# Kernel tuning notes

Measured on AMD Instinct MI355X. Metric: run time of the kernel, lower is better.

The kernel has to match this reference:

```python
import jax, jax.numpy as jnp
import numpy as np

B, N, FEAT, HID, OUT = 128, 64, 4, 256, 4
E = N * (N - 1)  # fully-connected graph, no self-loops


def _onehot_rel():
    # off-diagonal (recv, send) pairs, matching NRI's encode_onehot construction
    recv, send = np.where(~np.eye(N, dtype=bool))
    rel_rec = np.eye(N, dtype=np.float32)[recv]   # [E, N]
    rel_send = np.eye(N, dtype=np.float32)[send]  # [E, N]
    return jnp.asarray(rel_rec), jnp.asarray(rel_send)


def setup_inputs() -> dict:
    key = jax.random.key(0)
    ks = jax.random.split(key, 8)
    rel_rec, rel_send = _onehot_rel()

    def xavier(k, shape):
        fan_in, fan_out = shape
        lim = (6.0 / (fan_in + fan_out)) ** 0.5
        return jax.random.uniform(k, shape, jnp.float32, -lim, lim)

    return {
        "inputs": jax.random.normal(ks[0], (B, N, FEAT), jnp.float32),
        "edges": jax.random.normal(ks[1], (B, E, 2), jnp.float32),  # unused by forward (as in source)
        "rel_rec": rel_rec,
        "rel_send": rel_send,
        "W_msg1": xavier(ks[2], (2 * FEAT, HID)), "b_msg1": jnp.zeros((HID,), jnp.float32),
        "W_msg2": xavier(ks[3], (HID, HID)),      "b_msg2": jnp.zeros((HID,), jnp.float32),
        "W_out1": xavier(ks[4], (FEAT + HID, HID)), "b_out1": jnp.zeros((HID,), jnp.float32),
        "W_out2": xavier(ks[5], (HID, HID)),      "b_out2": jnp.zeros((HID,), jnp.float32),
        "W_out3": xavier(ks[6], (HID, OUT)),      "b_out3": jnp.zeros((OUT,), jnp.float32),
    }


def reference(inputs, edges, rel_rec, rel_send,
              W_msg1, b_msg1, W_msg2, b_msg2,
              W_out1, b_out1, W_out2, b_out2, W_out3, b_out3):
    x = inputs.reshape(inputs.shape[0], inputs.shape[1], -1)  # [B, N, F]
    # gather node features to edges via one-hot matmuls (faithful to source)
    receivers = jnp.einsum('en,bnf->bef', rel_rec, x)   # [B, E, F]
    senders = jnp.einsum('en,bnf->bef', rel_send, x)    # [B, E, F]
    pre_msg = jnp.concatenate([receivers, senders], axis=-1)  # [B, E, 2F]
    # edge MLP (dropout_prob = 0.0 -> identity)
    msg = jax.nn.relu(pre_msg @ W_msg1 + b_msg1)
    msg = jax.nn.relu(msg @ W_msg2 + b_msg2)            # [B, E, HID]
    # scatter-aggregate back to nodes via rel_rec^T
    agg_msg = jnp.einsum('en,beh->bnh', rel_rec, msg)   # [B, N, HID]
    out = jnp.concatenate([x, agg_msg], axis=-1)        # [B, N, F+HID]
    out = jax.nn.relu(out @ W_out1 + b_out1)
    out = jax.nn.relu(out @ W_out2 + b_out2)
    out = out @ W_out3 + b_out3                          # [B, N, 4]
    return out
```

## Files before the change

kernel.cpp:

```cpp
#include <hip/hip_runtime.h>
#include <cstddef>

typedef _Float16 f16_t;
typedef _Float16 f16x8 __attribute__((ext_vector_type(8)));
typedef float    f32x4  __attribute__((ext_vector_type(4)));
typedef float    f32x16 __attribute__((ext_vector_type(16)));

static constexpr int NN = 64;
static constexpr int FF = 4;
static constexpr int HH = 256;


__device__ inline void pack_frag16(const float* __restrict__ src, f16_t* __restrict__ dst,
                                   int fid, int ksteps, int mode)
{
    if (fid >= ksteps * 1024) return;
    int lane = fid & 63;
    int nt   = (fid >> 6) & 15;
    int ks   = fid >> 10;
    int col  = nt * 16 + (lane & 15);
    int kb   = ks * 32 + (lane >> 4) * 8;
    #pragma unroll
    for (int j = 0; j < 8; ++j) {
        int k = kb + j;
        float v;
        if (mode == 0) {
            v = src[k * 256 + col];
        } else {
            if (k < 256)      v = src[(4 + k) * 256 + col];
            else if (k < 260) v = src[(k - 256) * 256 + col];
            else              v = 0.f;
        }
        dst[(size_t)fid * 8 + j] = (f16_t)v;
    }
}

__device__ inline void pack_frag32(const float* __restrict__ src, f16_t* __restrict__ dst,
                                   int fid)
{
    int lane = fid & 63;
    int nt   = (fid >> 6) & 7;
    int ks   = fid >> 9;
    int col  = nt * 32 + (lane & 31);
    int kb   = ks * 16 + (lane >> 5) * 8;
    #pragma unroll
    for (int j = 0; j < 8; ++j)
        dst[(size_t)fid * 8 + j] = (f16_t)src[(kb + j) * 256 + col];
}

__global__ void prep_all(const float* __restrict__ x,
                         const float* __restrict__ W_msg1,
                         const float* __restrict__ W_msg2,
                         const float* __restrict__ W_out1,
                         const float* __restrict__ W_out2,
                         f16_t* __restrict__ W2p, f16_t* __restrict__ W1op,
                         f16_t* __restrict__ W2op, f16_t* __restrict__ Vp)
{
    int bid = blockIdx.x, tid = threadIdx.x;
    if (bid < 32) {
        pack_frag32(W_msg2, W2p, bid * 256 + tid);
    } else if (bid < 68) {
        pack_frag16(W_out1, W1op, (bid - 32) * 256 + tid, 9, 1);
    } else if (bid < 100) {
        pack_frag16(W_out2, W2op, (bid - 68) * 256 + tid, 8, 0);
    } else {
        int gid  = (bid - 100) * 256 + tid;
        int rown = gid >> 5;
        int h0   = (gid & 31) * 8;
        float4 xv = ((const float4*)x)[rown];
        f16x8 o;
        #pragma unroll
        for (int u = 0; u < 8; ++u) {
            float s = xv.x * W_msg1[4 * HH + h0 + u] + xv.y * W_msg1[5 * HH + h0 + u]
                    + xv.z * W_msg1[6 * HH + h0 + u] + xv.w * W_msg1[7 * HH + h0 + u];
            o[u] = (f16_t)s;
        }
        *(f16x8*)(Vp + (size_t)rown * HH + h0) = o;
    }
}

__global__ __launch_bounds__(256, 2) void edge_kernel(
    const float* __restrict__ x,
    const float* __restrict__ W1,
    const float* __restrict__ b1,
    const f16_t* __restrict__ Vp,
    const f16_t* __restrict__ W2p,
    const float* __restrict__ b2,
    f16_t* __restrict__ innode)
{
    __shared__ __align__(16) char h1[128 * 512];
    __shared__ __align__(16) f16_t Utab[2][256];

    const int tid  = threadIdx.x;
    const int lane = tid & 63;
    const int w    = tid >> 6;
    const int b    = blockIdx.x >> 5;
    const int pr   = blockIdx.x & 31;
    const int i0   = pr * 2, i1 = i0 + 1;

    #pragma unroll
    for (int i = 0; i < 2; ++i) {
        int e    = tid + i * 256;
        int rs   = e >> 8;
        int h    = e & 255;
        int node = rs ? i1 : i0;
        const float* xr = x + (b * NN + node) * FF;
        float s = b1[h] + xr[0] * W1[h] + xr[1] * W1[HH + h]
                        + xr[2] * W1[2 * HH + h] + xr[3] * W1[3 * HH + h];
        Utab[rs][h] = (f16_t)s;
    }
    if (tid < 64) {
        int node = (tid < 32) ? i0 : i1;
        int c = tid & 31;
        float v = (c < 4) ? x[(b * NN + node) * FF + c] : 0.f;
        innode[(size_t)(b * NN + node) * 288 + 256 + c] = (f16_t)v;
    }
    __syncthreads();

    {
        const int hb = tid & 31;
        const int rg = tid >> 5;
        const int h0 = hb * 8;
        const int recv = (rg < 4) ? i0 : i1;
        const f16x8 fz = {};
        f16x8 u8 = *(const f16x8*)&Utab[rg >> 2][h0];
        const int j0 = (rg & 3) * 16;
        const f16x8* vrow = (const f16x8*)(Vp + (size_t)(b * NN + j0) * HH + h0);
        #pragma unroll
        for (int k = 0; k < 16; ++k) {
            int r = rg * 16 + k;
            f16x8 v8 = vrow[k * (HH / 8)];
            f16x8 hv = __builtin_elementwise_max(u8 + v8, fz);
            *(f16x8*)(h1 + r * 512 + (((hb ^ (r & 31)) & 31) << 4)) = hv;
        }
        if ((rg & 3) == (recv >> 4)) {
            int r = rg * 16 + (recv & 15);
            *(f16x8*)(h1 + r * 512 + (((hb ^ (r & 31)) & 31) << 4)) = fz;
        }
    }
    __syncthreads();

    const int ln = lane & 31;
    const int kh = lane >> 5;
    const int wn = w;

    float b2v[2];
    #pragma unroll
    for (int nt = 0; nt < 2; ++nt) b2v[nt] = b2[(wn * 2 + nt) * 32 + ln];

    f32x16 acc[4][2];
    #pragma unroll
    for (int mt = 0; mt < 4; ++mt)
        #pragma unroll
        for (int nt = 0; nt < 2; ++nt)
            #pragma unroll
            for (int e = 0; e < 16; ++e) acc[mt][nt][e] = b2v[nt];

    #pragma unroll
    for (int ks = 0; ks < 16; ++ks) {
        f16x8 bb[2];
        #pragma unroll
        for (int nt = 0; nt < 2; ++nt)
            bb[nt] = *(const f16x8*)(W2p + (size_t)((ks * 8 + wn * 2 + nt) * 64 + lane) * 8);
        #pragma unroll
        for (int mt = 0; mt < 4; ++mt) {
            int row = mt * 32 + ln;
            int c16 = (ks * 2 + kh) ^ (row & 31);
            f16x8 a = *(const f16x8*)(h1 + row * 512 + (c16 << 4));
            #pragma unroll
            for (int nt = 0; nt < 2; ++nt)
                acc[mt][nt] = __builtin_amdgcn_mfma_f32_32x32x16_f16(a, bb[nt], acc[mt][nt], 0, 0, 0);
        }
    }

    float s0[2] = {0.f, 0.f}, s1[2] = {0.f, 0.f};
    #pragma unroll
    for (int mt = 0; mt < 4; ++mt)
        #pragma unroll
        for (int nt = 0; nt < 2; ++nt) {
            float t = 0.f;
            #pragma unroll
            for (int e = 0; e < 16; ++e) t += fmaxf(acc[mt][nt][e], 0.f);
            if (mt < 2) s0[nt] += t; else s1[nt] += t;
        }
    #pragma unroll
    for (int nt = 0; nt < 2; ++nt) {
        s0[nt] += __shfl_xor(s0[nt], 32);
        s1[nt] += __shfl_xor(s1[nt], 32);
    }
    if (lane < 32) {
        #pragma unroll
        for (int nt = 0; nt < 2; ++nt) {
            float sub = fmaxf(b2v[nt], 0.f);
            int col = (wn * 2 + nt) * 32 + ln;
            innode[(size_t)(b * NN + i0) * 288 + col] = (f16_t)(s0[nt] - sub);
            innode[(size_t)(b * NN + i1) * 288 + col] = (f16_t)(s1[nt] - sub);
        }
    }
}

__global__ __launch_bounds__(256, 4) void node_kernel(
    const f16_t* __restrict__ innode,
    const f16_t* __restrict__ W1op,
    const float* __restrict__ bo1,
    const f16_t* __restrict__ W2op,
    const float* __restrict__ bo2,
    const float* __restrict__ W3,
    const float* __restrict__ bo3,
    float* __restrict__ out)
{
    __shared__ __align__(16) char bufA[16 * 640];
    __shared__ __align__(16) char bufB[16 * 512];
    __shared__ __align__(16) char bufC[16 * 528];

    const int tid  = threadIdx.x;
    const int lane = tid & 63;
    const int w    = tid >> 6;
    const int m0   = blockIdx.x * 16;
    const int lm   = lane & 15, lk = lane >> 4;

    for (int idx = tid; idx < 16 * 36; idx += 256) {
        int r = idx / 36, c = idx - r * 36;
        f16x8 v = *(const f16x8*)(innode + (size_t)(m0 + r) * 288 + c * 8);
        *(f16x8*)(bufA + ((r * 640 + c * 16) ^ ((r & 7) << 4))) = v;
    }
    __syncthreads();

    f32x4 acc1[4];
    #pragma unroll
    for (int nt = 0; nt < 4; ++nt) {
        float bias = bo1[(w * 4 + nt) * 16 + lm];
        acc1[nt] = (f32x4){bias, bias, bias, bias};
    }
    #pragma unroll
    for (int ks = 0; ks < 9; ++ks) {
        f16x8 a = *(const f16x8*)(bufA + ((lm * 640 + ks * 64 + lk * 16) ^ ((lm & 7) << 4)));
        #pragma unroll
        for (int nt = 0; nt < 4; ++nt) {
            f16x8 bb = *(const f16x8*)(W1op + (size_t)((ks * 16 + w * 4 + nt) * 64 + lane) * 8);
            acc1[nt] = __builtin_amdgcn_mfma_f32_16x16x32_f16(a, bb, acc1[nt], 0, 0, 0);
        }
    }
    #pragma unroll
    for (int nt = 0; nt < 4; ++nt) {
        int col = (w * 4 + nt) * 16 + lm;
        #pragma unroll
        for (int j = 0; j < 4; ++j) {
            int row = lk * 4 + j;
            float v = fmaxf(acc1[nt][j], 0.f);
            *(f16_t*)(bufB + ((row * 512 + col * 2) ^ ((row & 7) << 4))) = (f16_t)v;
        }
    }
    __syncthreads();

    f32x4 acc2[4];
    #pragma unroll
    for (int nt = 0; nt < 4; ++nt) {
        float bias = bo2[(w * 4 + nt) * 16 + lm];
        acc2[nt] = (f32x4){bias, bias, bias, bias};
    }
    #pragma unroll
    for (int ks = 0; ks < 8; ++ks) {
        f16x8 a = *(const f16x8*)(bufB + ((lm * 512 + ks * 64 + lk * 16) ^ ((lm & 7) << 4)));
        #pragma unroll
        for (int nt = 0; nt < 4; ++nt) {
            f16x8 bb = *(const f16x8*)(W2op + (size_t)((ks * 16 + w * 4 + nt) * 64 + lane) * 8);
            acc2[nt] = __builtin_amdgcn_mfma_f32_16x16x32_f16(a, bb, acc2[nt], 0, 0, 0);
        }
    }
    f16_t* c16 = (f16_t*)bufC;
    #pragma unroll
    for (int nt = 0; nt < 4; ++nt) {
        int col = (w * 4 + nt) * 16 + lm;
        #pragma unroll
        for (int j = 0; j < 4; ++j) {
            int row = lk * 4 + j;
            float v = fmaxf(acc2[nt][j], 0.f);
            c16[row * 264 + col] = (f16_t)v;
        }
    }
    __syncthreads();

    {
        int m = tid >> 4;
        int o = (tid >> 2) & 3;
        int q = tid & 3;
        const f16_t* crow = c16 + m * 264 + q * 64;
        float s = 0.f;
        int rot = (lane & 15) * 4;
        #pragma unroll 8
        for (int k = 0; k < 64; ++k) {
            int kk = (k + rot) & 63;
            s += (float)crow[kk] * W3[(q * 64 + kk) * 4 + o];
        }
        s += __shfl_xor(s, 1);
        s += __shfl_xor(s, 2);
        if (q == 0) out[(size_t)(m0 + m) * 4 + o] = s + bo3[o];
    }
}

extern "C" void kernel_launch(void* const* d_in, const int* in_sizes, int n_in,
                              void* d_out, int out_size, void* d_ws, size_t ws_size,
                              hipStream_t stream)
{
    (void)in_sizes; (void)n_in; (void)out_size; (void)ws_size;
    const float* x      = (const float*)d_in[0];
    const float* W_msg1 = (const float*)d_in[4];
    const float* b_msg1 = (const float*)d_in[5];
    const float* W_msg2 = (const float*)d_in[6];
    const float* b_msg2 = (const float*)d_in[7];
    const float* W_out1 = (const float*)d_in[8];
    const float* b_out1 = (const float*)d_in[9];
    const float* W_out2 = (const float*)d_in[10];
    const float* b_out2 = (const float*)d_in[11];
    const float* W_out3 = (const float*)d_in[12];
    const float* b_out3 = (const float*)d_in[13];
    float* out = (float*)d_out;

    char* ws = (char*)d_ws;
    f16_t* W2p    = (f16_t*)(ws + 0);
    f16_t* W1op   = (f16_t*)(ws + 131072);
    f16_t* W2op   = (f16_t*)(ws + 278528);
    f16_t* innode = (f16_t*)(ws + 409600);
    f16_t* Vp     = (f16_t*)(ws + 5128192);

    prep_all<<<1124, 256, 0, stream>>>(x, W_msg1, W_msg2, W_out1, W_out2,
                                       W2p, W1op, W2op, Vp);
    edge_kernel<<<4096, 256, 0, stream>>>(x, W_msg1, b_msg1, Vp, W2p, b_msg2, innode);
    node_kernel<<<512, 256, 0, stream>>>(innode, W1op, b_out1, W2op, b_out2,
                                         W_out3, b_out3, out);
}
```

Baseline: 95.59 us.

## Split edge-hidden build in K halves and overlap second half with MFMA

The first-layer hidden tile in LDS is now built for the first 128 columns only before the barrier. The second 128 columns are built inside the first half of the K loop, interleaved with the MFMAs, and a new barrier separates the two halves. W2 fragments are also prefetched one K step ahead in registers. The aim is to hide the global V loads and the LDS writes behind matrix work, at the cost of an extra barrier and more register pressure.

```diff
diff --git a/kernel.cpp b/kernel.cpp
--- a/kernel.cpp
+++ b/kernel.cpp
@@ -115,39 +115,43 @@
         float v = (c < 4) ? x[(b * NN + node) * FF + c] : 0.f;
         innode[(size_t)(b * NN + node) * 288 + 256 + c] = (f16_t)v;
     }
+
+    const int ln = lane & 31;
+    const int kh = lane >> 5;
+    const int wn = w;
+    f16x8 bbn0 = *(const f16x8*)(W2p + (size_t)((0 * 8 + wn * 2 + 0) * 64 + lane) * 8);
+    f16x8 bbn1 = *(const f16x8*)(W2p + (size_t)((0 * 8 + wn * 2 + 1) * 64 + lane) * 8);
+
+    const int hb = tid & 15;
+    const int rg = tid >> 4;
+    const int h0 = hb * 8;
+    const int rs = rg >> 3;
+    const int recv = rs ? i1 : i0;
+    const int j0 = (rg & 7) * 8;
+    const f16x8 fz = {};
+
     __syncthreads();
 
     {
-        const int hb = tid & 31;
-        const int rg = tid >> 5;
-        const int h0 = hb * 8;
-        const int recv = (rg < 4) ? i0 : i1;
-        const f16x8 fz = {};
-        f16x8 u8 = *(const f16x8*)&Utab[rg >> 2][h0];
-        const int j0 = (rg & 3) * 16;
+        f16x8 u8 = *(const f16x8*)&Utab[rs][h0];
         const f16x8* vrow = (const f16x8*)(Vp + (size_t)(b * NN + j0) * HH + h0);
         #pragma unroll
-        for (int k = 0; k < 16; ++k) {
-            int r = rg * 16 + k;
+        for (int k = 0; k < 8; ++k) {
+            int r = rg * 8 + k;
             f16x8 v8 = vrow[k * (HH / 8)];
             f16x8 hv = __builtin_elementwise_max(u8 + v8, fz);
             *(f16x8*)(h1 + r * 512 + (((hb ^ (r & 31)) & 31) << 4)) = hv;
         }
-        if ((rg & 3) == (recv >> 4)) {
-            int r = rg * 16 + (recv & 15);
+        if ((rg & 7) == (recv >> 3)) {
+            int r = rg * 8 + (recv & 7);
             *(f16x8*)(h1 + r * 512 + (((hb ^ (r & 31)) & 31) << 4)) = fz;
         }
     }
     __syncthreads();
 
-    const int ln = lane & 31;
-    const int kh = lane >> 5;
-    const int wn = w;
-
     float b2v[2];
     #pragma unroll
     for (int nt = 0; nt < 2; ++nt) b2v[nt] = b2[(wn * 2 + nt) * 32 + ln];
-
     f32x16 acc[4][2];
     #pragma unroll
     for (int mt = 0; mt < 4; ++mt)
@@ -156,20 +160,56 @@
             #pragma unroll
             for (int e = 0; e < 16; ++e) acc[mt][nt][e] = b2v[nt];
 
-    #pragma unroll
-    for (int ks = 0; ks < 16; ++ks) {
-        f16x8 bb[2];
-        #pragma unroll
-        for (int nt = 0; nt < 2; ++nt)
-            bb[nt] = *(const f16x8*)(W2p + (size_t)((ks * 8 + wn * 2 + nt) * 64 + lane) * 8);
-        #pragma unroll
-        for (int mt = 0; mt < 4; ++mt) {
-            int row = mt * 32 + ln;
-            int c16 = (ks * 2 + kh) ^ (row & 31);
-            f16x8 a = *(const f16x8*)(h1 + row * 512 + (c16 << 4));
+    {
+        f16x8 u8B = *(const f16x8*)&Utab[rs][128 + h0];
+        const f16x8* vrowB = (const f16x8*)(Vp + (size_t)(b * NN + j0) * HH + 128 + h0);
+        #pragma unroll
+        for (int ks = 0; ks < 8; ++ks) {
+            f16x8 bb0 = bbn0, bb1 = bbn1;
+            if (ks < 7) {
+                bbn0 = *(const f16x8*)(W2p + (size_t)(((ks + 1) * 8 + wn * 2 + 0) * 64 + lane) * 8);
+                bbn1 = *(const f16x8*)(W2p + (size_t)(((ks + 1) * 8 + wn * 2 + 1) * 64 + lane) * 8);
+            }
+            {
+                int r = rg * 8 + ks;
+                f16x8 v8 = vrowB[ks * (HH / 8)];
+                f16x8 hv = __builtin_elementwise_max(u8B + v8, fz);
+                *(f16x8*)(h1 + r * 512 + ((((16 + hb) ^ (r & 31)) & 31) << 4)) = hv;
+            }
             #pragma unroll
-            for (int nt = 0; nt < 2; ++nt)
-                acc[mt][nt] = __builtin_amdgcn_mfma_f32_32x32x16_f16(a, bb[nt], acc[mt][nt], 0, 0, 0);
+            for (int mt = 0; mt < 4; ++mt) {
+                int row = mt * 32 + ln;
+                int c16 = (ks * 2 + kh) ^ (row & 31);
+                f16x8 a = *(const f16x8*)(h1 + row * 512 + (c16 << 4));
+                acc[mt][0] = __builtin_amdgcn_mfma_f32_32x32x16_f16(a, bb0, acc[mt][0], 0, 0, 0);
+                acc[mt][1] = __builtin_amdgcn_mfma_f32_32x32x16_f16(a, bb1, acc[mt][1], 0, 0, 0);
+            }
+        }
+        if ((rg & 7) == (recv >> 3)) {
+            int r = rg * 8 + (recv & 7);
+            *(f16x8*)(h1 + r * 512 + ((((16 + hb) ^ (r & 31)) & 31) << 4)) = fz;
+        }
+    }
+    __syncthreads();
+
+    {
+        f16x8 bbn0b = *(const f16x8*)(W2p + (size_t)((8 * 8 + wn * 2 + 0) * 64 + lane) * 8);
+        f16x8 bbn1b = *(const f16x8*)(W2p + (size_t)((8 * 8 + wn * 2 + 1) * 64 + lane) * 8);
+        #pragma unroll
+        for (int ks = 8; ks < 16; ++ks) {
+            f16x8 bb0 = bbn0b, bb1 = bbn1b;
+            if (ks < 15) {
+                bbn0b = *(const f16x8*)(W2p + (size_t)(((ks + 1) * 8 + wn * 2 + 0) * 64 + lane) * 8);
+                bbn1b = *(const f16x8*)(W2p + (size_t)(((ks + 1) * 8 + wn * 2 + 1) * 64 + lane) * 8);
+            }
+            #pragma unroll
+            for (int mt = 0; mt < 4; ++mt) {
+                int row = mt * 32 + ln;
+                int c16 = (ks * 2 + kh) ^ (row & 31);
+                f16x8 a = *(const f16x8*)(h1 + row * 512 + (c16 << 4));
+                acc[mt][0] = __builtin_amdgcn_mfma_f32_32x32x16_f16(a, bb0, acc[mt][0], 0, 0, 0);
+                acc[mt][1] = __builtin_amdgcn_mfma_f32_32x32x16_f16(a, bb1, acc[mt][1], 0, 0, 0);
+            }
         }
     }
 
```

Result: slower. 99.21 us (+3.8%).

## Warp-specialize edge kernel into double-buffered producer/consumer persistent blocks

Applied to the files above, without the earlier changes.

The edge kernel becomes persistent: 256 blocks of 512 threads each process 16 node-pair tiles. Four producer waves build the next ReLU'd first-layer tile into one of two LDS buffers while four consumer waves run the MFMA second layer on the previous tile. The per-node receiver term U and the x tail of innode move into the prep kernel, and W2 fragments are prefetched one k-step ahead. The aim is to overlap global loads and LDS fills with matrix work. The cost is only 256 blocks, a barrier per stage, and 128KB of LDS per block, which may limit occupancy to one block per CU.

```diff
diff --git a/kernel.cpp b/kernel.cpp
--- a/kernel.cpp
+++ b/kernel.cpp
@@ -50,11 +50,13 @@
 
 __global__ void prep_all(const float* __restrict__ x,
                          const float* __restrict__ W_msg1,
+                         const float* __restrict__ b_msg1,
                          const float* __restrict__ W_msg2,
                          const float* __restrict__ W_out1,
                          const float* __restrict__ W_out2,
                          f16_t* __restrict__ W2p, f16_t* __restrict__ W1op,
-                         f16_t* __restrict__ W2op, f16_t* __restrict__ Vp)
+                         f16_t* __restrict__ W2op, f16_t* __restrict__ Vp,
+                         f16_t* __restrict__ Up, f16_t* __restrict__ innode)
 {
     int bid = blockIdx.x, tid = threadIdx.x;
     if (bid < 32) {
@@ -66,136 +68,142 @@
     } else {
         int gid  = (bid - 100) * 256 + tid;
         int rown = gid >> 5;
-        int h0   = (gid & 31) * 8;
+        int hb   = gid & 31;
+        int h0   = hb * 8;
         float4 xv = ((const float4*)x)[rown];
-        f16x8 o;
+        f16x8 ov, ou;
         #pragma unroll
         for (int u = 0; u < 8; ++u) {
-            float s = xv.x * W_msg1[4 * HH + h0 + u] + xv.y * W_msg1[5 * HH + h0 + u]
-                    + xv.z * W_msg1[6 * HH + h0 + u] + xv.w * W_msg1[7 * HH + h0 + u];
-            o[u] = (f16_t)s;
-        }
-        *(f16x8*)(Vp + (size_t)rown * HH + h0) = o;
-    }
-}
-
-__global__ __launch_bounds__(256, 2) void edge_kernel(
-    const float* __restrict__ x,
-    const float* __restrict__ W1,
-    const float* __restrict__ b1,
+            int h = h0 + u;
+            float sv = xv.x * W_msg1[4 * HH + h] + xv.y * W_msg1[5 * HH + h]
+                     + xv.z * W_msg1[6 * HH + h] + xv.w * W_msg1[7 * HH + h];
+            float su = b_msg1[h]
+                     + xv.x * W_msg1[0 * HH + h] + xv.y * W_msg1[1 * HH + h]
+                     + xv.z * W_msg1[2 * HH + h] + xv.w * W_msg1[3 * HH + h];
+            ov[u] = (f16_t)sv;
+            ou[u] = (f16_t)su;
+        }
+        *(f16x8*)(Vp + (size_t)rown * HH + h0) = ov;
+        *(f16x8*)(Up + (size_t)rown * HH + h0) = ou;
+        float xt = (hb < 4) ? ((const float*)&xv)[hb] : 0.f;
+        innode[(size_t)rown * 288 + 256 + hb] = (f16_t)xt;
+    }
+}
+
+__global__ __launch_bounds__(512, 2) void edge_kernel(
     const f16_t* __restrict__ Vp,
+    const f16_t* __restrict__ Up,
     const f16_t* __restrict__ W2p,
     const float* __restrict__ b2,
     f16_t* __restrict__ innode)
 {
-    __shared__ __align__(16) char h1[128 * 512];
-    __shared__ __align__(16) f16_t Utab[2][256];
+    __shared__ __align__(16) char h1[2][128 * 512];
 
     const int tid  = threadIdx.x;
     const int lane = tid & 63;
     const int w    = tid >> 6;
-    const int b    = blockIdx.x >> 5;
-    const int pr   = blockIdx.x & 31;
-    const int i0   = pr * 2, i1 = i0 + 1;
-
-    #pragma unroll
-    for (int i = 0; i < 2; ++i) {
-        int e    = tid + i * 256;
-        int rs   = e >> 8;
-        int h    = e & 255;
-        int node = rs ? i1 : i0;
-        const float* xr = x + (b * NN + node) * FF;
-        float s = b1[h] + xr[0] * W1[h] + xr[1] * W1[HH + h]
-                        + xr[2] * W1[2 * HH + h] + xr[3] * W1[3 * HH + h];
-        Utab[rs][h] = (f16_t)s;
-    }
-    if (tid < 64) {
-        int node = (tid < 32) ? i0 : i1;
-        int c = tid & 31;
-        float v = (c < 4) ? x[(b * NN + node) * FF + c] : 0.f;
-        innode[(size_t)(b * NN + node) * 288 + 256 + c] = (f16_t)v;
-    }
-    __syncthreads();
-
-    {
-        const int hb = tid & 31;
-        const int rg = tid >> 5;
-        const int h0 = hb * 8;
-        const int recv = (rg < 4) ? i0 : i1;
-        const f16x8 fz = {};
-        f16x8 u8 = *(const f16x8*)&Utab[rg >> 2][h0];
-        const int j0 = (rg & 3) * 16;
-        const f16x8* vrow = (const f16x8*)(Vp + (size_t)(b * NN + j0) * HH + h0);
-        #pragma unroll
-        for (int k = 0; k < 16; ++k) {
-            int r = rg * 16 + k;
-            f16x8 v8 = vrow[k * (HH / 8)];
-            f16x8 hv = __builtin_elementwise_max(u8 + v8, fz);
-            *(f16x8*)(h1 + r * 512 + (((hb ^ (r & 31)) & 31) << 4)) = hv;
-        }
-        if ((rg & 3) == (recv >> 4)) {
-            int r = rg * 16 + (recv & 15);
-            *(f16x8*)(h1 + r * 512 + (((hb ^ (r & 31)) & 31) << 4)) = fz;
-        }
-    }
-    __syncthreads();
+    const bool producer = (w < 4);
+    const int tile0 = blockIdx.x * 16;
 
     const int ln = lane & 31;
     const int kh = lane >> 5;
-    const int wn = w;
-
+    const int wn = w & 3;
     float b2v[2];
     #pragma unroll
     for (int nt = 0; nt < 2; ++nt) b2v[nt] = b2[(wn * 2 + nt) * 32 + ln];
 
-    f32x16 acc[4][2];
-    #pragma unroll
-    for (int mt = 0; mt < 4; ++mt)
-        #pragma unroll
-        for (int nt = 0; nt < 2; ++nt)
-            #pragma unroll
-            for (int e = 0; e < 16; ++e) acc[mt][nt][e] = b2v[nt];
-
-    #pragma unroll
-    for (int ks = 0; ks < 16; ++ks) {
-        f16x8 bb[2];
-        #pragma unroll
-        for (int nt = 0; nt < 2; ++nt)
-            bb[nt] = *(const f16x8*)(W2p + (size_t)((ks * 8 + wn * 2 + nt) * 64 + lane) * 8);
-        #pragma unroll
-        for (int mt = 0; mt < 4; ++mt) {
-            int row = mt * 32 + ln;
-            int c16 = (ks * 2 + kh) ^ (row & 31);
-            f16x8 a = *(const f16x8*)(h1 + row * 512 + (c16 << 4));
-            #pragma unroll
-            for (int nt = 0; nt < 2; ++nt)
-                acc[mt][nt] = __builtin_amdgcn_mfma_f32_32x32x16_f16(a, bb[nt], acc[mt][nt], 0, 0, 0);
-        }
-    }
-
-    float s0[2] = {0.f, 0.f}, s1[2] = {0.f, 0.f};
-    #pragma unroll
-    for (int mt = 0; mt < 4; ++mt)
-        #pragma unroll
-        for (int nt = 0; nt < 2; ++nt) {
-            float t = 0.f;
-            #pragma unroll
-            for (int e = 0; e < 16; ++e) t += fmaxf(acc[mt][nt][e], 0.f);
-            if (mt < 2) s0[nt] += t; else s1[nt] += t;
-        }
-    #pragma unroll
-    for (int nt = 0; nt < 2; ++nt) {
-        s0[nt] += __shfl_xor(s0[nt], 32);
-        s1[nt] += __shfl_xor(s1[nt], 32);
-    }
-    if (lane < 32) {
-        #pragma unroll
-        for (int nt = 0; nt < 2; ++nt) {
-            float sub = fmaxf(b2v[nt], 0.f);
-            int col = (wn * 2 + nt) * 32 + ln;
-            innode[(size_t)(b * NN + i0) * 288 + col] = (f16_t)(s0[nt] - sub);
-            innode[(size_t)(b * NN + i1) * 288 + col] = (f16_t)(s1[nt] - sub);
-        }
+    const int hb = tid & 15;
+    const int rg = tid >> 4;
+    const int j0 = (rg & 7) * 8;
+    const f16x8 fz = {};
+
+    for (int s = 0; s <= 16; ++s) {
+        if (producer && s < 16) {
+            const int t  = tile0 + s;
+            const int b  = t >> 5;
+            const int pr = t & 31;
+            const int i0 = pr * 2, i1 = i0 + 1;
+            const int recv = (rg < 8) ? i0 : i1;
+            char* wb = h1[s & 1];
+            const f16x8* vrow = (const f16x8*)(Vp + (size_t)(b * NN + j0) * HH);
+            const f16x8* urow = (const f16x8*)(Up + (size_t)(b * NN + recv) * HH);
+            #pragma unroll
+            for (int half = 0; half < 2; ++half) {
+                const int cb = half * 16 + hb;
+                f16x8 u8 = urow[half * 16 + hb];
+                #pragma unroll
+                for (int k = 0; k < 8; ++k) {
+                    int r = rg * 8 + k;
+                    f16x8 v8 = vrow[k * 32 + half * 16 + hb];
+                    f16x8 hv = __builtin_elementwise_max(u8 + v8, fz);
+                    *(f16x8*)(wb + r * 512 + (((cb ^ (r & 31)) & 31) << 4)) = hv;
+                }
+                if ((rg & 7) == (recv >> 3)) {
+                    int r = rg * 8 + (recv & 7);
+                    *(f16x8*)(wb + r * 512 + (((cb ^ (r & 31)) & 31) << 4)) = fz;
+                }
+            }
+        }
+        if (!producer && s > 0) {
+            const int t  = tile0 + s - 1;
+            const int b  = t >> 5;
+            const int pr = t & 31;
+            const int i0 = pr * 2, i1 = i0 + 1;
+            const char* rb = h1[(s - 1) & 1];
+
+            f32x16 acc[4][2];
+            #pragma unroll
+            for (int mt = 0; mt < 4; ++mt)
+                #pragma unroll
+                for (int nt = 0; nt < 2; ++nt)
+                    #pragma unroll
+                    for (int e = 0; e < 16; ++e) acc[mt][nt][e] = b2v[nt];
+
+            f16x8 bbn0 = *(const f16x8*)(W2p + (size_t)((wn * 2 + 0) * 64 + lane) * 8);
+            f16x8 bbn1 = *(const f16x8*)(W2p + (size_t)((wn * 2 + 1) * 64 + lane) * 8);
+            #pragma unroll
+            for (int ks = 0; ks < 16; ++ks) {
+                f16x8 bb0 = bbn0, bb1 = bbn1;
+                if (ks < 15) {
+                    bbn0 = *(const f16x8*)(W2p + (size_t)(((ks + 1) * 8 + wn * 2 + 0) * 64 + lane) * 8);
+                    bbn1 = *(const f16x8*)(W2p + (size_t)(((ks + 1) * 8 + wn * 2 + 1) * 64 + lane) * 8);
+                }
+                #pragma unroll
+                for (int mt = 0; mt < 4; ++mt) {
+                    int row = mt * 32 + ln;
+                    int c16 = (ks * 2 + kh) ^ (row & 31);
+                    f16x8 a = *(const f16x8*)(rb + row * 512 + (c16 << 4));
+                    acc[mt][0] = __builtin_amdgcn_mfma_f32_32x32x16_f16(a, bb0, acc[mt][0], 0, 0, 0);
+                    acc[mt][1] = __builtin_amdgcn_mfma_f32_32x32x16_f16(a, bb1, acc[mt][1], 0, 0, 0);
+                }
+            }
+
+            float s0[2] = {0.f, 0.f}, s1[2] = {0.f, 0.f};
+            #pragma unroll
+            for (int mt = 0; mt < 4; ++mt)
+                #pragma unroll
+                for (int nt = 0; nt < 2; ++nt) {
+                    float tacc = 0.f;
+                    #pragma unroll
+                    for (int e = 0; e < 16; ++e) tacc += fmaxf(acc[mt][nt][e], 0.f);
+                    if (mt < 2) s0[nt] += tacc; else s1[nt] += tacc;
+                }
+            #pragma unroll
+            for (int nt = 0; nt < 2; ++nt) {
+                s0[nt] += __shfl_xor(s0[nt], 32);
+                s1[nt] += __shfl_xor(s1[nt], 32);
+            }
+            if (lane < 32) {
+                #pragma unroll
+                for (int nt = 0; nt < 2; ++nt) {
+                    float sub = fmaxf(b2v[nt], 0.f);
+                    int col = (wn * 2 + nt) * 32 + ln;
+                    innode[(size_t)(b * NN + i0) * 288 + col] = (f16_t)(s0[nt] - sub);
+                    innode[(size_t)(b * NN + i1) * 288 + col] = (f16_t)(s1[nt] - sub);
+                }
+            }
+        }
+        __syncthreads();
     }
 }
 
@@ -323,10 +331,11 @@
     f16_t* W2op   = (f16_t*)(ws + 278528);
     f16_t* innode = (f16_t*)(ws + 409600);
     f16_t* Vp     = (f16_t*)(ws + 5128192);
-
-    prep_all<<<1124, 256, 0, stream>>>(x, W_msg1, W_msg2, W_out1, W_out2,
-                                       W2p, W1op, W2op, Vp);
-    edge_kernel<<<4096, 256, 0, stream>>>(x, W_msg1, b_msg1, Vp, W2p, b_msg2, innode);
+    f16_t* Up     = (f16_t*)(ws + 9322496);
+
+    prep_all<<<1124, 256, 0, stream>>>(x, W_msg1, b_msg1, W_msg2, W_out1, W_out2,
+                                       W2p, W1op, W2op, Vp, Up, innode);
+    edge_kernel<<<256, 512, 0, stream>>>(Vp, Up, W2p, b_msg2, innode);
     node_kernel<<<512, 256, 0, stream>>>(innode, W1op, b_out1, W2op, b_out2,
                                          W_out3, b_out3, out);
 }
```

Result: slower. 154.5 us (+61.6%).

## Prefetch W2 fragments in edge kernel, packed ReLU-sum, and 32-row node tiles

Applied to the files above, without the earlier changes.

The edge kernel's second GEMM now loads the next k-step's weight fragments before issuing the current MFMAs, a software prefetch meant to hide global load latency. The ReLU-and-sum epilogue uses 2-wide float vectors so the compiler can emit packed max/add instructions. The node kernel switches from 16 rows per 256-thread block to 32 rows per 512-thread block, so each weight fragment load is shared by two row tiles. The cost is more registers in the edge loop, and half as many node blocks, which may reduce parallelism.

```diff
diff --git a/kernel.cpp b/kernel.cpp
--- a/kernel.cpp
+++ b/kernel.cpp
@@ -3,6 +3,7 @@
 
 typedef _Float16 f16_t;
 typedef _Float16 f16x8 __attribute__((ext_vector_type(8)));
+typedef float    f32x2  __attribute__((ext_vector_type(2)));
 typedef float    f32x4  __attribute__((ext_vector_type(4)));
 typedef float    f32x16 __attribute__((ext_vector_type(16)));
 
@@ -156,33 +157,51 @@
             #pragma unroll
             for (int e = 0; e < 16; ++e) acc[mt][nt][e] = b2v[nt];
 
+    f16x8 bbn0 = *(const f16x8*)(W2p + (size_t)((wn * 2 + 0) * 64 + lane) * 8);
+    f16x8 bbn1 = *(const f16x8*)(W2p + (size_t)((wn * 2 + 1) * 64 + lane) * 8);
     #pragma unroll
     for (int ks = 0; ks < 16; ++ks) {
-        f16x8 bb[2];
-        #pragma unroll
-        for (int nt = 0; nt < 2; ++nt)
-            bb[nt] = *(const f16x8*)(W2p + (size_t)((ks * 8 + wn * 2 + nt) * 64 + lane) * 8);
+        f16x8 bb0 = bbn0, bb1 = bbn1;
+        if (ks < 15) {
+            bbn0 = *(const f16x8*)(W2p + (size_t)(((ks + 1) * 8 + wn * 2 + 0) * 64 + lane) * 8);
+            bbn1 = *(const f16x8*)(W2p + (size_t)(((ks + 1) * 8 + wn * 2 + 1) * 64 + lane) * 8);
+        }
         #pragma unroll
         for (int mt = 0; mt < 4; ++mt) {
             int row = mt * 32 + ln;
             int c16 = (ks * 2 + kh) ^ (row & 31);
             f16x8 a = *(const f16x8*)(h1 + row * 512 + (c16 << 4));
+            acc[mt][0] = __builtin_amdgcn_mfma_f32_32x32x16_f16(a, bb0, acc[mt][0], 0, 0, 0);
+            acc[mt][1] = __builtin_amdgcn_mfma_f32_32x32x16_f16(a, bb1, acc[mt][1], 0, 0, 0);
+        }
+    }
+
+    const f32x2 zz = {0.f, 0.f};
+    f32x2 p0[2] = {zz, zz}, p1[2] = {zz, zz};
+    #pragma unroll
+    for (int mt = 0; mt < 4; ++mt)
+        #pragma unroll
+        for (int nt = 0; nt < 2; ++nt) {
+            f32x2 t = zz;
             #pragma unroll
-            for (int nt = 0; nt < 2; ++nt)
-                acc[mt][nt] = __builtin_amdgcn_mfma_f32_32x32x16_f16(a, bb[nt], acc[mt][nt], 0, 0, 0);
-        }
-    }
-
-    float s0[2] = {0.f, 0.f}, s1[2] = {0.f, 0.f};
-    #pragma unroll
-    for (int mt = 0; mt < 4; ++mt)
-        #pragma unroll
-        for (int nt = 0; nt < 2; ++nt) {
-            float t = 0.f;
-            #pragma unroll
-            for (int e = 0; e < 16; ++e) t += fmaxf(acc[mt][nt][e], 0.f);
-            if (mt < 2) s0[nt] += t; else s1[nt] += t;
-        }
+            for (int h = 0; h < 8; ++h) {
+                f32x2 e;
+                switch (h) {
+                    case 0: e = __builtin_shufflevector(acc[mt][nt], acc[mt][nt], 0, 1); break;
+                    case 1: e = __builtin_shufflevector(acc[mt][nt], acc[mt][nt], 2, 3); break;
+                    case 2: e = __builtin_shufflevector(acc[mt][nt], acc[mt][nt], 4, 5); break;
+                    case 3: e = __builtin_shufflevector(acc[mt][nt], acc[mt][nt], 6, 7); break;
+                    case 4: e = __builtin_shufflevector(acc[mt][nt], acc[mt][nt], 8, 9); break;
+                    case 5: e = __builtin_shufflevector(acc[mt][nt], acc[mt][nt], 10, 11); break;
+                    case 6: e = __builtin_shufflevector(acc[mt][nt], acc[mt][nt], 12, 13); break;
+                    default: e = __builtin_shufflevector(acc[mt][nt], acc[mt][nt], 14, 15); break;
+                }
+                t += __builtin_elementwise_max(e, zz);
+            }
+            if (mt < 2) p0[nt] += t; else p1[nt] += t;
+        }
+    float s0[2] = {p0[0].x + p0[0].y, p0[1].x + p0[1].y};
+    float s1[2] = {p1[0].x + p1[0].y, p1[1].x + p1[1].y};
     #pragma unroll
     for (int nt = 0; nt < 2; ++nt) {
         s0[nt] += __shfl_xor(s0[nt], 32);
@@ -199,7 +218,7 @@
     }
 }
 
-__global__ __launch_bounds__(256, 4) void node_kernel(
+__global__ __launch_bounds__(512, 2) void node_kernel(
     const f16_t* __restrict__ innode,
     const f16_t* __restrict__ W1op,
     const float* __restrict__ bo1,
@@ -209,17 +228,19 @@
     const float* __restrict__ bo3,
     float* __restrict__ out)
 {
-    __shared__ __align__(16) char bufA[16 * 640];
-    __shared__ __align__(16) char bufB[16 * 512];
-    __shared__ __align__(16) char bufC[16 * 528];
+    __shared__ __align__(16) char bufA[32 * 640];
+    __shared__ __align__(16) char bufB[32 * 512];
+    __shared__ __align__(16) char bufC[32 * 528];
 
     const int tid  = threadIdx.x;
     const int lane = tid & 63;
     const int w    = tid >> 6;
-    const int m0   = blockIdx.x * 16;
+    const int m0   = blockIdx.x * 32;
     const int lm   = lane & 15, lk = lane >> 4;
-
-    for (int idx = tid; idx < 16 * 36; idx += 256) {
+    const int mt   = w >> 2;
+    const int ntq  = w & 3;
+
+    for (int idx = tid; idx < 32 * 36; idx += 512) {
         int r = idx / 36, c = idx - r * 36;
         f16x8 v = *(const f16x8*)(innode + (size_t)(m0 + r) * 288 + c * 8);
         *(f16x8*)(bufA + ((r * 640 + c * 16) ^ ((r & 7) << 4))) = v;
@@ -229,24 +250,25 @@
     f32x4 acc1[4];
     #pragma unroll
     for (int nt = 0; nt < 4; ++nt) {
-        float bias = bo1[(w * 4 + nt) * 16 + lm];
+        float bias = bo1[(ntq * 4 + nt) * 16 + lm];
         acc1[nt] = (f32x4){bias, bias, bias, bias};
     }
     #pragma unroll
     for (int ks = 0; ks < 9; ++ks) {
-        f16x8 a = *(const f16x8*)(bufA + ((lm * 640 + ks * 64 + lk * 16) ^ ((lm & 7) << 4)));
+        int r = mt * 16 + lm;
+        f16x8 a = *(const f16x8*)(bufA + ((r * 640 + ks * 64 + lk * 16) ^ ((r & 7) << 4)));
         #pragma unroll
         for (int nt = 0; nt < 4; ++nt) {
-            f16x8 bb = *(const f16x8*)(W1op + (size_t)((ks * 16 + w * 4 + nt) * 64 + lane) * 8);
+            f16x8 bb = *(const f16x8*)(W1op + (size_t)((ks * 16 + ntq * 4 + nt) * 64 + lane) * 8);
             acc1[nt] = __builtin_amdgcn_mfma_f32_16x16x32_f16(a, bb, acc1[nt], 0, 0, 0);
         }
     }
     #pragma unroll
     for (int nt = 0; nt < 4; ++nt) {
-        int col = (w * 4 + nt) * 16 + lm;
+        int col = (ntq * 4 + nt) * 16 + lm;
         #pragma unroll
         for (int j = 0; j < 4; ++j) {
-            int row = lk * 4 + j;
+            int row = mt * 16 + lk * 4 + j;
             float v = fmaxf(acc1[nt][j], 0.f);
             *(f16_t*)(bufB + ((row * 512 + col * 2) ^ ((row & 7) << 4))) = (f16_t)v;
         }
@@ -256,25 +278,26 @@
     f32x4 acc2[4];
     #pragma unroll
     for (int nt = 0; nt < 4; ++nt) {
-        float bias = bo2[(w * 4 + nt) * 16 + lm];
+        float bias = bo2[(ntq * 4 + nt) * 16 + lm];
         acc2[nt] = (f32x4){bias, bias, bias, bias};
     }
     #pragma unroll
     for (int ks = 0; ks < 8; ++ks) {
-        f16x8 a = *(const f16x8*)(bufB + ((lm * 512 + ks * 64 + lk * 16) ^ ((lm & 7) << 4)));
+        int r = mt * 16 + lm;
+        f16x8 a = *(const f16x8*)(bufB + ((r * 512 + ks * 64 + lk * 16) ^ ((r & 7) << 4)));
         #pragma unroll
         for (int nt = 0; nt < 4; ++nt) {
-            f16x8 bb = *(const f16x8*)(W2op + (size_t)((ks * 16 + w * 4 + nt) * 64 + lane) * 8);
+            f16x8 bb = *(const f16x8*)(W2op + (size_t)((ks * 16 + ntq * 4 + nt) * 64 + lane) * 8);
             acc2[nt] = __builtin_amdgcn_mfma_f32_16x16x32_f16(a, bb, acc2[nt], 0, 0, 0);
         }
     }
     f16_t* c16 = (f16_t*)bufC;
     #pragma unroll
     for (int nt = 0; nt < 4; ++nt) {
-        int col = (w * 4 + nt) * 16 + lm;
+        int col = (ntq * 4 + nt) * 16 + lm;
         #pragma unroll
         for (int j = 0; j < 4; ++j) {
-            int row = lk * 4 + j;
+            int row = mt * 16 + lk * 4 + j;
             float v = fmaxf(acc2[nt][j], 0.f);
             c16[row * 264 + col] = (f16_t)v;
         }
@@ -327,6 +350,6 @@
     prep_all<<<1124, 256, 0, stream>>>(x, W_msg1, W_msg2, W_out1, W_out2,
                                        W2p, W1op, W2op, Vp);
     edge_kernel<<<4096, 256, 0, stream>>>(x, W_msg1, b_msg1, Vp, W2p, b_msg2, innode);
-    node_kernel<<<512, 256, 0, stream>>>(innode, W1op, b_out1, W2op, b_out2,
+    node_kernel<<<256, 512, 0, stream>>>(innode, W1op, b_out1, W2op, b_out2,
                                          W_out3, b_out3, out);
 }
```

New measurement: 95.86 us. Within noise of the previous version (+0.3%).
